# Performance work log

Hardware: AMD Instinct MI355X
Metric: run time of the kernel (lower is better)

The kernel has to match this reference:

```python
import jax, jax.numpy as jnp
import numpy as np
import math

OMEGA_0 = 30.0
LAYER_SIZES = [3, 256, 256, 256, 256, 3]
N_POINTS = 524288


def _siren_params(key):
    """SIREN initialization matching the original module."""
    keys = jax.random.split(key, len(LAYER_SIZES) - 1)
    params = {}
    for i in range(len(LAYER_SIZES) - 1):
        in_dim, out_dim = LAYER_SIZES[i], LAYER_SIZES[i + 1]
        k = keys[i]
        bound = (1.0 / in_dim) if i == 0 else (math.sqrt(6.0 / in_dim) / OMEGA_0)
        W = jax.random.uniform(k, (out_dim, in_dim), minval=-bound, maxval=bound, dtype=jnp.float32)
        b = jax.random.uniform(k, (out_dim,), minval=-1e-6, maxval=1e-6, dtype=jnp.float32)
        params[f"W{i}"] = W
        params[f"b{i}"] = b
    return params


def setup_inputs() -> dict:
    key = jax.random.key(0)
    kx, kp = jax.random.split(key)
    # coordinates in [-1, 1], typical SIREN input domain
    x = jax.random.uniform(kx, (N_POINTS, 3), minval=-1.0, maxval=1.0, dtype=jnp.float32)
    inp = {"x": x}
    inp.update(_siren_params(kp))
    return inp


def reference(x, W0, b0, W1, b1, W2, b2, W3, b3, W4, b4):
    # First layer: sin(omega_0 * (W0 @ x + b0)), batched over rows of x.
    h = jnp.sin(OMEGA_0 * (jnp.einsum("ni,oi->no", x, W0) + b0))
    # Hidden layers: sin(W @ h + b)
    h = jnp.sin(jnp.einsum("ni,oi->no", h, W1) + b1)
    h = jnp.sin(jnp.einsum("ni,oi->no", h, W2) + b2)
    h = jnp.sin(jnp.einsum("ni,oi->no", h, W3) + b3)
    # Final layer: linear, no activation.
    out = jnp.einsum("ni,oi->no", h, W4) + b4
    return out
```

## Files before the change

### kernel.cpp

```cpp
#include <hip/hip_runtime.h>
#include <stdint.h>


typedef float    f32x4  __attribute__((ext_vector_type(4)));
typedef float    f32x16 __attribute__((ext_vector_type(16)));
typedef short    s16x8  __attribute__((ext_vector_type(8)));
typedef uint32_t u32x2  __attribute__((ext_vector_type(2)));
typedef uint32_t u32x4  __attribute__((ext_vector_type(4)));

#define INV2PI 0.15915494309189535f
#define L0SCALE 4.774648292756860f
#define W4OFF 196608

__device__ __forceinline__ uint16_t f32_to_bf16(float f) {
    uint32_t u = __builtin_bit_cast(uint32_t, f);
    u += 0x7FFFu + ((u >> 16) & 1u);
    return (uint16_t)(u >> 16);
}
__device__ __forceinline__ uint32_t pack_bf16x2(float lo, float hi) {
#if __has_builtin(__builtin_amdgcn_cvt_pk_bf16_f32)
    auto v = __builtin_amdgcn_cvt_pk_bf16_f32(lo, hi);
    return __builtin_bit_cast(uint32_t, v);
#else
    uint32_t a = __builtin_bit_cast(uint32_t, lo);
    uint32_t b = __builtin_bit_cast(uint32_t, hi);
    a += 0x7FFFu + ((a >> 16) & 1u);
    b += 0x7FFFu + ((b >> 16) & 1u);
    return (a >> 16) | (b & 0xFFFF0000u);
#endif
}
__device__ __forceinline__ float sin_rev(float r) {
    return __builtin_amdgcn_sinf(r);
}

__global__ void convert_weights(const float* __restrict__ W1,
                                const float* __restrict__ W2,
                                const float* __restrict__ W3,
                                const float* __restrict__ W4,
                                uint16_t* __restrict__ wsb) {
    int tid = blockIdx.x * blockDim.x + threadIdx.x;
    if (tid < 196608) {
        int l = tid >> 16;
        int r = tid & 65535;
        int c = r >> 8;
        int k = r & 255;
        const float* W = (l == 0) ? W1 : (l == 1) ? W2 : W3;
        int kc16 = k >> 4, cb = c >> 5;
        int lane = (c & 31) | (((k >> 3) & 1) << 5);
        int j = k & 7;
        wsb[(((l * 16 + kc16) * 8 + cb) * 64 + lane) * 8 + j] =
            f32_to_bf16(W[c * 256 + k] * INV2PI);
    } else if (tid < 200704) {
        int e = tid - 196608;
        int kk = e >> 9, lane = (e >> 3) & 63, j = e & 7;
        int n16 = lane & 15, q = lane >> 4;
        float v = (n16 < 3) ? W4[n16 * 256 + kk * 32 + q * 8 + j] : 0.0f;
        wsb[W4OFF + (kk * 64 + lane) * 8 + j] = f32_to_bf16(v);
    }
}

__global__ __launch_bounds__(128, 2) void siren_main(
    const float* __restrict__ x,
    const float* __restrict__ W0, const float* __restrict__ b0,
    const float* __restrict__ b1, const float* __restrict__ b2,
    const float* __restrict__ b3,
    const float* __restrict__ b4,
    const uint16_t* __restrict__ Wb,
    float* __restrict__ out)
{
    __shared__ uint16_t h_lds[2048 * 8];

    const int tid  = threadIdx.x;
    const int lane = tid & 63;
    const int wid  = tid >> 6;
    const int n16  = lane & 15;
    const int q    = lane >> 4;
    const int lam  = lane & 31;
    const int hi   = lane >> 5;
    const int p0   = blockIdx.x * 64;

    s16x8 Wbuf[2][2][4];
    #pragma unroll
    for (int kc2 = 0; kc2 < 2; ++kc2)
        #pragma unroll
        for (int t = 0; t < 4; ++t)
            Wbuf[0][kc2][t] = *(const s16x8*)(Wb +
                ((kc2 * 8 + wid * 4 + t) * 64 + lane) * 8);

    {
        float xv[4][3];
        #pragma unroll
        for (int rt = 0; rt < 4; ++rt) {
            const float* xp = x + (p0 + rt * 16 + n16) * 3;
            xv[rt][0] = xp[0]; xv[rt][1] = xp[1]; xv[rt][2] = xp[2];
        }
        #pragma unroll
        for (int oo = 0; oo < 4; ++oo) {
            const int octet = wid * 16 + oo * 4 + q;
            const float* w0r = W0 + octet * 24;
            float wv[24];
            #pragma unroll
            for (int i = 0; i < 24; ++i) wv[i] = w0r[i] * L0SCALE;
            float bb[8];
            #pragma unroll
            for (int i = 0; i < 8; ++i) bb[i] = b0[octet * 8 + i] * L0SCALE;
            #pragma unroll
            for (int rt = 0; rt < 4; ++rt) {
                u32x4 pk;
                #pragma unroll
                for (int j2 = 0; j2 < 4; ++j2) {
                    float za = wv[(2*j2  )*3+0] * xv[rt][0] +
                               wv[(2*j2  )*3+1] * xv[rt][1] +
                               wv[(2*j2  )*3+2] * xv[rt][2] + bb[2*j2];
                    float zb = wv[(2*j2+1)*3+0] * xv[rt][0] +
                               wv[(2*j2+1)*3+1] * xv[rt][1] +
                               wv[(2*j2+1)*3+2] * xv[rt][2] + bb[2*j2+1];
                    pk[j2] = pack_bf16x2(sin_rev(za), sin_rev(zb));
                }
                const int pt = rt * 16 + n16;
                const int u = ((octet >> 1) * 2 + (pt >> 5)) * 64
                            + (octet & 1) * 32 + (pt & 31);
                *(u32x4*)&h_lds[u * 8] = pk;
            }
        }
    }
    __syncthreads();

    #pragma unroll
    for (int l = 0; l < 3; ++l) {
        const float* bl = (l == 0) ? b1 : (l == 1) ? b2 : b3;

        f32x16 acc[4][2];
        #pragma unroll
        for (int t = 0; t < 4; ++t)
            #pragma unroll
            for (int g = 0; g < 4; ++g) {
                f32x4 bv = *(const f32x4*)&bl[wid * 128 + t * 32 + g * 8 + hi * 4];
                bv *= INV2PI;
                #pragma unroll
                for (int i = 0; i < 4; ++i) {
                    acc[t][0][g * 4 + i] = bv[i];
                    acc[t][1][g * 4 + i] = bv[i];
                }
            }

        #pragma unroll
        for (int kp = 0; kp < 8; ++kp) {
            const int cur = kp & 1, nxt = cur ^ 1;
            if (kp < 7) {
                #pragma unroll
                for (int kc2 = 0; kc2 < 2; ++kc2)
                    #pragma unroll
                    for (int t = 0; t < 4; ++t)
                        Wbuf[nxt][kc2][t] = *(const s16x8*)(Wb +
                            (((l * 16 + kp * 2 + 2 + kc2) * 8 + wid * 4 + t) * 64 + lane) * 8);
            } else if (l < 2) {
                #pragma unroll
                for (int kc2 = 0; kc2 < 2; ++kc2)
                    #pragma unroll
                    for (int t = 0; t < 4; ++t)
                        Wbuf[nxt][kc2][t] = *(const s16x8*)(Wb +
                            ((((l + 1) * 16 + kc2) * 8 + wid * 4 + t) * 64 + lane) * 8);
            }
            #pragma unroll
            for (int kc2 = 0; kc2 < 2; ++kc2) {
                const int kc16 = kp * 2 + kc2;
                s16x8 hf[2];
                #pragma unroll
                for (int s = 0; s < 2; ++s)
                    hf[s] = *(const s16x8*)&h_lds[((kc16 * 2 + s) * 64 + lane) * 8];
                #pragma unroll
                for (int t = 0; t < 4; ++t)
                    #pragma unroll
                    for (int s = 0; s < 2; ++s)
                        acc[t][s] = __builtin_amdgcn_mfma_f32_32x32x16_bf16(
                            Wbuf[cur][kc2][t], hf[s], acc[t][s], 0, 0, 0);
            }
        }
        __syncthreads();

        uint32_t* hw = (uint32_t*)h_lds;
        #pragma unroll
        for (int t = 0; t < 4; ++t)
            #pragma unroll
            for (int s = 0; s < 2; ++s)
                #pragma unroll
                for (int g = 0; g < 4; ++g) {
                    float v0 = sin_rev(acc[t][s][g * 4 + 0]);
                    float v1 = sin_rev(acc[t][s][g * 4 + 1]);
                    float v2 = sin_rev(acc[t][s][g * 4 + 2]);
                    float v3 = sin_rev(acc[t][s][g * 4 + 3]);
                    const int kc16p = wid * 8 + t * 2 + (g >> 1);
                    const int u = (kc16p * 2 + s) * 64 + (g & 1) * 32 + lam;
                    u32x2 w2 = { pack_bf16x2(v0, v1), pack_bf16x2(v2, v3) };
                    *(u32x2*)&hw[u * 4 + hi * 2] = w2;
                }
        __syncthreads();
    }

    {
        float bb4 = (n16 < 3) ? b4[n16] : 0.0f;
        s16x8 w4f[8];
        #pragma unroll
        for (int kk = 0; kk < 8; ++kk)
            w4f[kk] = *(const s16x8*)(Wb + W4OFF + (kk * 64 + lane) * 8);
        #pragma unroll
        for (int rt2 = 0; rt2 < 2; ++rt2) {
            f32x4 accF = { bb4, bb4, bb4, bb4 };
            #pragma unroll
            for (int kk = 0; kk < 8; ++kk) {
                const int u = ((kk * 2 + (q >> 1)) * 2 + wid) * 64
                            + (q & 1) * 32 + rt2 * 16 + n16;
                s16x8 af = *(const s16x8*)&h_lds[u * 8];
                accF = __builtin_amdgcn_mfma_f32_16x16x32_bf16(af, w4f[kk], accF, 0, 0, 0);
            }
            if (n16 < 3) {
                #pragma unroll
                for (int r = 0; r < 4; ++r)
                    out[(p0 + wid * 32 + rt2 * 16 + q * 4 + r) * 3 + n16] = accF[r];
            }
        }
    }
}

extern "C" void kernel_launch(void* const* d_in, const int* in_sizes, int n_in,
                              void* d_out, int out_size, void* d_ws, size_t ws_size,
                              hipStream_t stream) {
    const float* x  = (const float*)d_in[0];
    const float* W0 = (const float*)d_in[1];
    const float* b0 = (const float*)d_in[2];
    const float* W1 = (const float*)d_in[3];
    const float* b1 = (const float*)d_in[4];
    const float* W2 = (const float*)d_in[5];
    const float* b2 = (const float*)d_in[6];
    const float* W3 = (const float*)d_in[7];
    const float* b3 = (const float*)d_in[8];
    const float* W4 = (const float*)d_in[9];
    const float* b4 = (const float*)d_in[10];
    float* outp     = (float*)d_out;
    uint16_t* wsb   = (uint16_t*)d_ws;

    hipLaunchKernelGGL(convert_weights, dim3(784), dim3(256), 0, stream,
                       W1, W2, W3, W4, wsb);
    hipLaunchKernelGGL(siren_main, dim3(8192), dim3(128), 0, stream,
                       x, W0, b0, b1, b2, b3, b4, wsb, outp);
}
```

Measured before the change: 336.9 us.

## Split point columns across four waves per block and fuse final layer into epilogue

Each block now uses four waves instead of two. Every wave handles one 128-channel output half and one 32-point half, so each wave keeps half as many accumulators and the kernel can target three blocks per CU. The last hidden layer no longer writes to LDS for a separate MFMA output layer. Its sine outputs are multiplied directly with the fp32 W4 rows, reduced across lanes with shuffles and across waves through LDS, and then the bias is added. The risks are that each wave now reads the weight fragments on its own, doubling global/L2 weight traffic per block, and that W4 is read many times in scalar fp32.

```diff
diff --git a/kernel.cpp b/kernel.cpp
--- a/kernel.cpp
+++ b/kernel.cpp
@@ -10,7 +10,6 @@
 
 #define INV2PI 0.15915494309189535f
 #define L0SCALE 4.774648292756860f
-#define W4OFF 196608
 
 __device__ __forceinline__ uint16_t f32_to_bf16(float f) {
     uint32_t u = __builtin_bit_cast(uint32_t, f);
@@ -36,35 +35,26 @@
 __global__ void convert_weights(const float* __restrict__ W1,
                                 const float* __restrict__ W2,
                                 const float* __restrict__ W3,
-                                const float* __restrict__ W4,
                                 uint16_t* __restrict__ wsb) {
     int tid = blockIdx.x * blockDim.x + threadIdx.x;
-    if (tid < 196608) {
-        int l = tid >> 16;
-        int r = tid & 65535;
-        int c = r >> 8;
-        int k = r & 255;
-        const float* W = (l == 0) ? W1 : (l == 1) ? W2 : W3;
-        int kc16 = k >> 4, cb = c >> 5;
-        int lane = (c & 31) | (((k >> 3) & 1) << 5);
-        int j = k & 7;
-        wsb[(((l * 16 + kc16) * 8 + cb) * 64 + lane) * 8 + j] =
-            f32_to_bf16(W[c * 256 + k] * INV2PI);
-    } else if (tid < 200704) {
-        int e = tid - 196608;
-        int kk = e >> 9, lane = (e >> 3) & 63, j = e & 7;
-        int n16 = lane & 15, q = lane >> 4;
-        float v = (n16 < 3) ? W4[n16 * 256 + kk * 32 + q * 8 + j] : 0.0f;
-        wsb[W4OFF + (kk * 64 + lane) * 8 + j] = f32_to_bf16(v);
-    }
-}
-
-__global__ __launch_bounds__(128, 2) void siren_main(
+    int l = tid >> 16;
+    int r = tid & 65535;
+    int c = r >> 8;
+    int k = r & 255;
+    const float* W = (l == 0) ? W1 : (l == 1) ? W2 : W3;
+    int kc16 = k >> 4, cb = c >> 5;
+    int lane = (c & 31) | (((k >> 3) & 1) << 5);
+    int j = k & 7;
+    wsb[(((l * 16 + kc16) * 8 + cb) * 64 + lane) * 8 + j] =
+        f32_to_bf16(W[c * 256 + k] * INV2PI);
+}
+
+__global__ __launch_bounds__(256, 3) void siren_main(
     const float* __restrict__ x,
     const float* __restrict__ W0, const float* __restrict__ b0,
     const float* __restrict__ b1, const float* __restrict__ b2,
     const float* __restrict__ b3,
-    const float* __restrict__ b4,
+    const float* __restrict__ W4, const float* __restrict__ b4,
     const uint16_t* __restrict__ Wb,
     float* __restrict__ out)
 {
@@ -73,6 +63,8 @@
     const int tid  = threadIdx.x;
     const int lane = tid & 63;
     const int wid  = tid >> 6;
+    const int cw   = wid >> 1;
+    const int pw   = wid & 1;
     const int n16  = lane & 15;
     const int q    = lane >> 4;
     const int lam  = lane & 31;
@@ -85,7 +77,7 @@
         #pragma unroll
         for (int t = 0; t < 4; ++t)
             Wbuf[0][kc2][t] = *(const s16x8*)(Wb +
-                ((kc2 * 8 + wid * 4 + t) * 64 + lane) * 8);
+                ((kc2 * 8 + cw * 4 + t) * 64 + lane) * 8);
 
     {
         float xv[4][3];
@@ -95,8 +87,8 @@
             xv[rt][0] = xp[0]; xv[rt][1] = xp[1]; xv[rt][2] = xp[2];
         }
         #pragma unroll
-        for (int oo = 0; oo < 4; ++oo) {
-            const int octet = wid * 16 + oo * 4 + q;
+        for (int oo = 0; oo < 2; ++oo) {
+            const int octet = wid * 8 + oo * 4 + q;
             const float* w0r = W0 + octet * 24;
             float wv[24];
             #pragma unroll
@@ -130,18 +122,15 @@
     for (int l = 0; l < 3; ++l) {
         const float* bl = (l == 0) ? b1 : (l == 1) ? b2 : b3;
 
-        f32x16 acc[4][2];
+        f32x16 acc[4];
         #pragma unroll
         for (int t = 0; t < 4; ++t)
             #pragma unroll
             for (int g = 0; g < 4; ++g) {
-                f32x4 bv = *(const f32x4*)&bl[wid * 128 + t * 32 + g * 8 + hi * 4];
+                f32x4 bv = *(const f32x4*)&bl[cw * 128 + t * 32 + g * 8 + hi * 4];
                 bv *= INV2PI;
                 #pragma unroll
-                for (int i = 0; i < 4; ++i) {
-                    acc[t][0][g * 4 + i] = bv[i];
-                    acc[t][1][g * 4 + i] = bv[i];
-                }
+                for (int i = 0; i < 4; ++i) acc[t][g * 4 + i] = bv[i];
             }
 
         #pragma unroll
@@ -153,71 +142,78 @@
                     #pragma unroll
                     for (int t = 0; t < 4; ++t)
                         Wbuf[nxt][kc2][t] = *(const s16x8*)(Wb +
-                            (((l * 16 + kp * 2 + 2 + kc2) * 8 + wid * 4 + t) * 64 + lane) * 8);
+                            (((l * 16 + kp * 2 + 2 + kc2) * 8 + cw * 4 + t) * 64 + lane) * 8);
             } else if (l < 2) {
                 #pragma unroll
                 for (int kc2 = 0; kc2 < 2; ++kc2)
                     #pragma unroll
                     for (int t = 0; t < 4; ++t)
                         Wbuf[nxt][kc2][t] = *(const s16x8*)(Wb +
-                            ((((l + 1) * 16 + kc2) * 8 + wid * 4 + t) * 64 + lane) * 8);
+                            ((((l + 1) * 16 + kc2) * 8 + cw * 4 + t) * 64 + lane) * 8);
             }
             #pragma unroll
             for (int kc2 = 0; kc2 < 2; ++kc2) {
                 const int kc16 = kp * 2 + kc2;
-                s16x8 hf[2];
-                #pragma unroll
-                for (int s = 0; s < 2; ++s)
-                    hf[s] = *(const s16x8*)&h_lds[((kc16 * 2 + s) * 64 + lane) * 8];
+                s16x8 hf = *(const s16x8*)&h_lds[((kc16 * 2 + pw) * 64 + lane) * 8];
                 #pragma unroll
                 for (int t = 0; t < 4; ++t)
-                    #pragma unroll
-                    for (int s = 0; s < 2; ++s)
-                        acc[t][s] = __builtin_amdgcn_mfma_f32_32x32x16_bf16(
-                            Wbuf[cur][kc2][t], hf[s], acc[t][s], 0, 0, 0);
+                    acc[t] = __builtin_amdgcn_mfma_f32_32x32x16_bf16(
+                        Wbuf[cur][kc2][t], hf, acc[t], 0, 0, 0);
             }
         }
         __syncthreads();
 
-        uint32_t* hw = (uint32_t*)h_lds;
-        #pragma unroll
-        for (int t = 0; t < 4; ++t)
-            #pragma unroll
-            for (int s = 0; s < 2; ++s)
+        if (l < 2) {
+            uint32_t* hw = (uint32_t*)h_lds;
+            #pragma unroll
+            for (int t = 0; t < 4; ++t)
                 #pragma unroll
                 for (int g = 0; g < 4; ++g) {
-                    float v0 = sin_rev(acc[t][s][g * 4 + 0]);
-                    float v1 = sin_rev(acc[t][s][g * 4 + 1]);
-                    float v2 = sin_rev(acc[t][s][g * 4 + 2]);
-                    float v3 = sin_rev(acc[t][s][g * 4 + 3]);
-                    const int kc16p = wid * 8 + t * 2 + (g >> 1);
-                    const int u = (kc16p * 2 + s) * 64 + (g & 1) * 32 + lam;
+                    float v0 = sin_rev(acc[t][g * 4 + 0]);
+                    float v1 = sin_rev(acc[t][g * 4 + 1]);
+                    float v2 = sin_rev(acc[t][g * 4 + 2]);
+                    float v3 = sin_rev(acc[t][g * 4 + 3]);
+                    const int kc16p = cw * 8 + t * 2 + (g >> 1);
+                    const int u = (kc16p * 2 + pw) * 64 + (g & 1) * 32 + lam;
                     u32x2 w2 = { pack_bf16x2(v0, v1), pack_bf16x2(v2, v3) };
                     *(u32x2*)&hw[u * 4 + hi * 2] = w2;
                 }
-        __syncthreads();
-    }
-
-    {
-        float bb4 = (n16 < 3) ? b4[n16] : 0.0f;
-        s16x8 w4f[8];
-        #pragma unroll
-        for (int kk = 0; kk < 8; ++kk)
-            w4f[kk] = *(const s16x8*)(Wb + W4OFF + (kk * 64 + lane) * 8);
-        #pragma unroll
-        for (int rt2 = 0; rt2 < 2; ++rt2) {
-            f32x4 accF = { bb4, bb4, bb4, bb4 };
-            #pragma unroll
-            for (int kk = 0; kk < 8; ++kk) {
-                const int u = ((kk * 2 + (q >> 1)) * 2 + wid) * 64
-                            + (q & 1) * 32 + rt2 * 16 + n16;
-                s16x8 af = *(const s16x8*)&h_lds[u * 8];
-                accF = __builtin_amdgcn_mfma_f32_16x16x32_bf16(af, w4f[kk], accF, 0, 0, 0);
-            }
-            if (n16 < 3) {
-                #pragma unroll
-                for (int r = 0; r < 4; ++r)
-                    out[(p0 + wid * 32 + rt2 * 16 + q * 4 + r) * 3 + n16] = accF[r];
+            __syncthreads();
+        } else {
+            float po0 = 0.f, po1 = 0.f, po2 = 0.f;
+            #pragma unroll
+            for (int t = 0; t < 4; ++t)
+                #pragma unroll
+                for (int g = 0; g < 4; ++g) {
+                    f32x4 sv;
+                    #pragma unroll
+                    for (int i = 0; i < 4; ++i)
+                        sv[i] = sin_rev(acc[t][g * 4 + i]);
+                    const int base = cw * 128 + t * 32 + g * 8 + hi * 4;
+                    f32x4 w0v = *(const f32x4*)&W4[0 * 256 + base];
+                    f32x4 w1v = *(const f32x4*)&W4[1 * 256 + base];
+                    f32x4 w2v = *(const f32x4*)&W4[2 * 256 + base];
+                    #pragma unroll
+                    for (int i = 0; i < 4; ++i) {
+                        po0 += w0v[i] * sv[i];
+                        po1 += w1v[i] * sv[i];
+                        po2 += w2v[i] * sv[i];
+                    }
+                }
+            po0 += __shfl_xor(po0, 32, 64);
+            po1 += __shfl_xor(po1, 32, 64);
+            po2 += __shfl_xor(po2, 32, 64);
+            float* red = (float*)h_lds;
+            if (hi == 0) {
+                const int pt = pw * 32 + lam;
+                red[cw * 192 + pt * 3 + 0] = po0;
+                red[cw * 192 + pt * 3 + 1] = po1;
+                red[cw * 192 + pt * 3 + 2] = po2;
+            }
+            __syncthreads();
+            if (tid < 192) {
+                const int o = tid - (tid / 3) * 3;
+                out[p0 * 3 + tid] = red[tid] + red[192 + tid] + b4[o];
             }
         }
     }
@@ -240,8 +236,8 @@
     float* outp     = (float*)d_out;
     uint16_t* wsb   = (uint16_t*)d_ws;
 
-    hipLaunchKernelGGL(convert_weights, dim3(784), dim3(256), 0, stream,
-                       W1, W2, W3, W4, wsb);
-    hipLaunchKernelGGL(siren_main, dim3(8192), dim3(128), 0, stream,
-                       x, W0, b0, b1, b2, b3, b4, wsb, outp);
-}
+    hipLaunchKernelGGL(convert_weights, dim3(768), dim3(256), 0, stream,
+                       W1, W2, W3, wsb);
+    hipLaunchKernelGGL(siren_main, dim3(8192), dim3(256), 0, stream,
+                       x, W0, b0, b1, b2, b3, W4, b4, wsb, outp);
+}
```

After: 370.4 us. 9.9% more time.
